# Optimization experiments

Measured on AMD Instinct MI355X. Metric: run time of the kernel, lower is better.

## Reference

```python
import jax, jax.numpy as jnp
import numpy as np

NUM_HEADS = 16


def setup_inputs() -> dict:
    key = jax.random.key(0)
    k1, k2, k3, k4 = jax.random.split(key, 4)
    B, N, C = 4, 2048, 1024
    x = jax.random.normal(k1, (B, N, C), dtype=jnp.float32)
    g_info = jax.random.normal(k2, (2, 4, C), dtype=jnp.float32)
    qkv_w = jax.random.normal(k3, (3 * C, C), dtype=jnp.float32) * 0.02
    proj_w = jax.random.normal(k4, (C, C), dtype=jnp.float32) * 0.02
    proj_b = jnp.zeros((C,), dtype=jnp.float32)
    return {"x": x, "g_info": g_info, "qkv_w": qkv_w, "proj_w": proj_w, "proj_b": proj_b}


def reference(x, g_info, qkv_w, proj_w, proj_b):
    B, N, C = x.shape
    H = NUM_HEADS
    D = C // H
    scale = D ** -0.5
    # qkv projection (no bias): [B,N,3C] -> [B,N,3,H,D]
    qkv = (x @ qkv_w.T).reshape(B, N, 3, H, D)
    q, k, v = qkv[:, :, 0], qkv[:, :, 1], qkv[:, :, 2]  # each [B,N,H,D]
    # global-info fusion: g_info[0] -> (4,H,D); rows = q_g, k_g, v_g, t_g
    gl = g_info[0].reshape(4, H, D)
    q_g = gl[0][None, None]  # [1,1,H,D]
    k_g = gl[1][None, None]
    # NOTE: source computes min/max rescaled q_g/k_g but they are dead code;
    # the attention actually uses the unscaled additive fusion below.
    q_fused = q + q_g
    k_fused = k + k_g
    # memory_efficient_attention(q,k,v): softmax(q k^T / sqrt(D)) v
    attn = jnp.einsum("bqhd,bkhd->bhqk", q_fused, k_fused) * scale
    attn = jax.nn.softmax(attn, axis=-1)
    out = jnp.einsum("bhqk,bkhd->bqhd", attn, v).reshape(B, N, C)
    out = out @ proj_w.T + proj_b
    return (out, g_info[1:])
```

## Files before the change

### kernel.cpp

```cpp
#include <hip/hip_runtime.h>

typedef _Float16 h4 __attribute__((ext_vector_type(4)));
typedef _Float16 h8 __attribute__((ext_vector_type(8)));
typedef __fp16 fp16x2 __attribute__((ext_vector_type(2)));
typedef float f4 __attribute__((ext_vector_type(4)));
typedef float f16v __attribute__((ext_vector_type(16)));

#define MFMA16(a,b,c) __builtin_amdgcn_mfma_f32_16x16x32_f16(a, b, c, 0, 0, 0)
#define MFMA32(a,b,c) __builtin_amdgcn_mfma_f32_32x32x16_f16(a, b, c, 0, 0, 0)
#define EXP2(x) __builtin_amdgcn_exp2f(x)

__device__ __forceinline__ void gload_lds16(const _Float16* g, _Float16* l) {
    __builtin_amdgcn_global_load_lds((const __attribute__((address_space(1))) void*)g,
                                     (__attribute__((address_space(3))) void*)l, 16, 0, 0);
}

__device__ __forceinline__ void half_swap(float v, float& a, float& b) {
    unsigned x = __float_as_uint(v), y = x;
    asm("v_permlane32_swap_b32 %0, %1" : "+v"(x), "+v"(y));
    a = __uint_as_float(x); b = __uint_as_float(y);
}

__device__ __forceinline__ h8 ldfrag_sw(const _Float16* S, int R, int kk, int kq) {
    int b = kk * 4 + kq;
    return *(const h8*)(S + R * 64 + ((b ^ (R & 7)) * 8));
}

__device__ __forceinline__ void gemm_main(const _Float16* __restrict__ A, const _Float16* __restrict__ B,
                                          int K, int tM, int tN, int tid,
                                          _Float16* As, _Float16* Bs, f4 acc[4][4]) {
    int lane = tid & 63, w = tid >> 6;
    int wm = w >> 1, wn = w & 1;
    int ln = lane & 15, kq = lane >> 4;
    int r = tid >> 3;
    int sb = tid & 7;

#define GSTAGE(buf, k0)                                                                     \
    {                                                                                       \
        _Pragma("unroll")                                                                   \
        for (int it = 0; it < 4; ++it) {                                                    \
            int row = r + it * 32;                                                          \
            int srcb = sb ^ (row & 7);                                                      \
            gload_lds16(A + (size_t)(tM * 128 + row) * K + (k0) + srcb * 8,                 \
                        As + (buf) * 8192 + ((tid & ~63) + it * 256) * 8);                  \
            gload_lds16(B + (size_t)(tN * 128 + row) * K + (k0) + srcb * 8,                 \
                        Bs + (buf) * 8192 + ((tid & ~63) + it * 256) * 8);                  \
        }                                                                                   \
    }

    GSTAGE(0, 0);
    __syncthreads();

    int cur = 0;
    for (int k0 = 0; k0 < K; k0 += 64) {
        if (k0 + 64 < K) GSTAGE(cur ^ 1, k0 + 64);

        const _Float16* Asc = As + cur * 8192;
        const _Float16* Bsc = Bs + cur * 8192;
        __builtin_amdgcn_s_setprio(1);
#pragma unroll
        for (int kk = 0; kk < 2; ++kk) {
            h8 af[4], bf[4];
#pragma unroll
            for (int mi = 0; mi < 4; ++mi) af[mi] = ldfrag_sw(Asc, wm * 64 + mi * 16 + ln, kk, kq);
#pragma unroll
            for (int ni = 0; ni < 4; ++ni) bf[ni] = ldfrag_sw(Bsc, wn * 64 + ni * 16 + ln, kk, kq);
#pragma unroll
            for (int mi = 0; mi < 4; ++mi)
#pragma unroll
                for (int ni = 0; ni < 4; ++ni) acc[mi][ni] = MFMA16(af[mi], bf[ni], acc[mi][ni]);
        }
        __builtin_amdgcn_s_setprio(0);
        __syncthreads();
        cur ^= 1;
    }
#undef GSTAGE
}

__global__ __launch_bounds__(256) void k_cvt3(const float* __restrict__ x, const float* __restrict__ wq,
                                              const float* __restrict__ wp, _Float16* __restrict__ xh,
                                              _Float16* __restrict__ wqh, _Float16* __restrict__ wph) {
    const int NX = 1048576, NQ = 393216, NP = 131072;
    int stride = gridDim.x * blockDim.x;
    for (int s = blockIdx.x * blockDim.x + threadIdx.x; s < NX + NQ + NP; s += stride) {
        const float* src;
        _Float16* dst;
        int off;
        if (s < NX) { src = x; dst = xh; off = s; }
        else if (s < NX + NQ) { src = wq; dst = wqh; off = s - NX; }
        else { src = wp; dst = wph; off = s - NX - NQ; }
        float4 a = ((const float4*)src)[off * 2];
        float4 b = ((const float4*)src)[off * 2 + 1];
        h8 r = {(_Float16)a.x, (_Float16)a.y, (_Float16)a.z, (_Float16)a.w,
                (_Float16)b.x, (_Float16)b.y, (_Float16)b.z, (_Float16)b.w};
        ((h8*)dst)[off] = r;
    }
}

__global__ __launch_bounds__(256) void k_qkv(const _Float16* __restrict__ A, const _Float16* __restrict__ B,
                                             const float* __restrict__ g, _Float16* __restrict__ Qf,
                                             _Float16* __restrict__ Kf, _Float16* __restrict__ Vt) {
    __shared__ __align__(16) _Float16 As[2 * 128 * 64];
    __shared__ __align__(16) _Float16 Bs[2 * 128 * 64];
    int tid = threadIdx.x;
    int tN = blockIdx.x, tM = blockIdx.y;
    int lane = tid & 63, w = tid >> 6;
    int wm = w >> 1, wn = w & 1;
    int ln = lane & 15, kq = lane >> 4;

    f4 acc[4][4] = {};
    gemm_main(A, B, 1024, tM, tN, tid, As, Bs, acc);

#pragma unroll
    for (int mi = 0; mi < 4; ++mi) {
#pragma unroll
        for (int ni = 0; ni < 4; ++ni) {
#pragma unroll
            for (int r = 0; r < 4; ++r) {
                int gr = tM * 128 + wm * 64 + mi * 16 + kq * 4 + r;
                int gc = tN * 128 + wn * 64 + ni * 16 + ln;
                float val = acc[mi][ni][r];
                int which = gc >> 10;
                int c = gc & 1023, h = c >> 6, d = c & 63;
                int b = gr >> 11, n = gr & 2047;
                int bh = b * 16 + h;
                if (which == 0) {
                    val = (val + g[c]) * 0.18033688f;
                    Qf[((size_t)bh * 2048 + n) * 64 + d] = (_Float16)val;
                } else if (which == 1) {
                    val += g[1024 + c];
                    Kf[((size_t)bh * 2048 + n) * 64 + d] = (_Float16)val;
                } else {
                    Vt[((size_t)bh * 64 + d) * 2048 + n] = (_Float16)val;
                }
            }
        }
    }
}

__global__ __launch_bounds__(256) void k_attn(const _Float16* __restrict__ Qf, const _Float16* __restrict__ Kf,
                                              const _Float16* __restrict__ Vt, _Float16* __restrict__ Oa) {
    __shared__ __align__(16) _Float16 KV[2][2][64 * 64];
    int tid = threadIdx.x;
    int qt = blockIdx.x, bh = blockIdx.y;
    int lane = tid & 63, w = tid >> 6;
    int l31 = lane & 31, hi = lane >> 5;
    const _Float16* Qb = Qf + (size_t)bh * 2048 * 64;
    const _Float16* Kb = Kf + (size_t)bh * 2048 * 64;
    const _Float16* Vb = Vt + (size_t)bh * 64 * 2048;
    int qrow0 = qt * 128 + w * 32;

    int srow = tid >> 3, sblk = tid & 7;
    int sblk0 = (sblk ^ (srow & 7)) * 8;

#define STAGE(bufi, kvc)                                                                     \
    {                                                                                        \
        _Float16* lk = &KV[bufi][0][0] + ((tid & ~63)) * 8;                                  \
        _Float16* lv = &KV[bufi][1][0] + ((tid & ~63)) * 8;                                  \
        gload_lds16(Kb + (size_t)((kvc) + srow) * 64 + sblk0, lk);                           \
        gload_lds16(Kb + (size_t)((kvc) + srow + 32) * 64 + sblk0, lk + 2048);               \
        gload_lds16(Vb + (size_t)srow * 2048 + (kvc) + sblk0, lv);                           \
        gload_lds16(Vb + (size_t)(srow + 32) * 2048 + (kvc) + sblk0, lv + 2048);             \
    }

    h8 qfr[4];
#pragma unroll
    for (int dc = 0; dc < 4; ++dc)
        qfr[dc] = *(const h8*)(Qb + (size_t)(qrow0 + l31) * 64 + dc * 16 + hi * 8);

    f16v o0 = {}, o1 = {};
    float l_run = 0.f;

    STAGE(0, 0);
    __syncthreads();

    int cur = 0;
    for (int kvc = 0; kvc < 2048; kvc += 64) {
        if (kvc + 64 < 2048) STAGE(cur ^ 1, kvc + 64);

        const _Float16* Klc = &KV[cur][0][0];
        const _Float16* Vlc = &KV[cur][1][0];
        int sw = l31 & 7;

        f16v s0, s1;
#pragma unroll
        for (int r = 0; r < 16; ++r) { s0[r] = -4.f; s1[r] = -4.f; }
        __builtin_amdgcn_s_setprio(1);
#pragma unroll
        for (int dc = 0; dc < 4; ++dc) {
            int cb = dc * 2 + hi;
            h8 kf0 = *(const h8*)&Klc[l31 * 64 + ((cb ^ sw) * 8)];
            h8 kf1 = *(const h8*)&Klc[(32 + l31) * 64 + ((cb ^ sw) * 8)];
            s0 = MFMA32(kf0, qfr[dc], s0);
            s1 = MFMA32(kf1, qfr[dc], s1);
        }
        __builtin_amdgcn_s_setprio(0);

        float ps0[16], ps1[16];
#pragma unroll
        for (int r = 0; r < 16; ++r) ps0[r] = EXP2(s0[r]);
#pragma unroll
        for (int r = 0; r < 16; ++r) ps1[r] = EXP2(s1[r]);

        float t[16];
#pragma unroll
        for (int i = 0; i < 16; ++i) t[i] = ps0[i] + ps1[i];
#pragma unroll
        for (int i = 0; i < 8; ++i) t[i] += t[i + 8];
#pragma unroll
        for (int i = 0; i < 4; ++i) t[i] += t[i + 4];
        l_run += (t[0] + t[1]) + (t[2] + t[3]);

        unsigned W[16];
#pragma unroll
        for (int i = 0; i < 8; ++i) {
            union { fp16x2 h; unsigned u; } a, b;
            a.h = __builtin_amdgcn_cvt_pkrtz(ps0[2 * i], ps0[2 * i + 1]);
            b.h = __builtin_amdgcn_cvt_pkrtz(ps1[2 * i], ps1[2 * i + 1]);
            W[i] = a.u;
            W[8 + i] = b.u;
        }

        __builtin_amdgcn_s_setprio(1);
#pragma unroll
        for (int t2 = 0; t2 < 2; ++t2) {
#pragma unroll
            for (int kcl = 0; kcl < 2; ++kcl) {
                unsigned w0 = W[t2 * 8 + kcl * 4 + 0], w1 = W[t2 * 8 + kcl * 4 + 1];
                unsigned w2 = W[t2 * 8 + kcl * 4 + 2], w3 = W[t2 * 8 + kcl * 4 + 3];
                asm("v_permlane32_swap_b32 %0, %1" : "+v"(w0), "+v"(w2));
                asm("v_permlane32_swap_b32 %0, %1" : "+v"(w1), "+v"(w3));
                union { unsigned u[4]; h8 v; } pf;
                pf.u[0] = w0; pf.u[1] = w1; pf.u[2] = w2; pf.u[3] = w3;
                int cb = (t2 * 2 + kcl) * 2 + hi;
                h8 vf0 = *(const h8*)&Vlc[l31 * 64 + ((cb ^ sw) * 8)];
                h8 vf1 = *(const h8*)&Vlc[(32 + l31) * 64 + ((cb ^ sw) * 8)];
                o0 = MFMA32(pf.v, vf0, o0);
                o1 = MFMA32(pf.v, vf1, o1);
            }
        }
        __builtin_amdgcn_s_setprio(0);

        __syncthreads();
        cur ^= 1;
    }
#undef STAGE

    float la, lb;
    half_swap(l_run, la, lb);
    float inv = 1.f / (la + lb);
    int b = bh >> 4, h = bh & 15;
#pragma unroll
    for (int r = 0; r < 16; ++r) {
        int qloc = (r & 3) + 8 * (r >> 2) + 4 * hi;
        float iv = __shfl(inv, qloc, 64);
        size_t base = ((size_t)b * 2048 + qrow0 + qloc) * 1024 + h * 64;
        Oa[base + l31] = (_Float16)(o0[r] * iv);
        Oa[base + 32 + l31] = (_Float16)(o1[r] * iv);
    }
}

__global__ __launch_bounds__(256) void k_proj(const _Float16* __restrict__ A, const _Float16* __restrict__ B,
                                              const float* __restrict__ bias, float* __restrict__ out) {
    __shared__ __align__(16) _Float16 As[2 * 128 * 64];
    __shared__ __align__(16) _Float16 Bs[2 * 128 * 64];
    int tid = threadIdx.x;
    int tN = blockIdx.x, tM = blockIdx.y;
    int lane = tid & 63, w = tid >> 6;
    int wm = w >> 1, wn = w & 1;
    int ln = lane & 15, kq = lane >> 4;

    f4 acc[4][4] = {};
    gemm_main(A, B, 1024, tM, tN, tid, As, Bs, acc);

#pragma unroll
    for (int mi = 0; mi < 4; ++mi) {
#pragma unroll
        for (int ni = 0; ni < 4; ++ni) {
#pragma unroll
            for (int r = 0; r < 4; ++r) {
                int gr = tM * 128 + wm * 64 + mi * 16 + kq * 4 + r;
                int gc = tN * 128 + wn * 64 + ni * 16 + ln;
                out[(size_t)gr * 1024 + gc] = acc[mi][ni][r] + bias[gc];
            }
        }
    }
}

__global__ __launch_bounds__(256) void k_tail(const float* __restrict__ g, float* __restrict__ out) {
    int i = blockIdx.x * 256 + threadIdx.x;
    out[i] = g[4096 + i];
}

extern "C" void kernel_launch(void* const* d_in, const int* in_sizes, int n_in,
                              void* d_out, int out_size, void* d_ws, size_t ws_size,
                              hipStream_t stream) {
    const float* x = (const float*)d_in[0];
    const float* g = (const float*)d_in[1];
    const float* wq = (const float*)d_in[2];
    const float* wp = (const float*)d_in[3];
    const float* pb = (const float*)d_in[4];
    float* out = (float*)d_out;

    _Float16* xh = (_Float16*)d_ws;
    _Float16* wqh = xh + 8388608;
    _Float16* wph = wqh + 3145728;
    _Float16* Qf = wph + 1048576;
    _Float16* Kf = Qf + 8388608;
    _Float16* Vt = Kf + 8388608;
    _Float16* Oa = xh;

    k_cvt3<<<2048, 256, 0, stream>>>(x, wq, wp, xh, wqh, wph);
    k_qkv<<<dim3(24, 64), 256, 0, stream>>>(xh, wqh, g, Qf, Kf, Vt);
    k_attn<<<dim3(16, 64), 256, 0, stream>>>(Qf, Kf, Vt, Oa);
    k_proj<<<dim3(8, 64), 256, 0, stream>>>(Oa, wph, pb, out);
    k_tail<<<16, 256, 0, stream>>>(g, out + 8388608);
}
```

Baseline: 230.9 us.

## Deepen GEMM pipeline to 4-stage ring with K=32 slices and single barrier

Restructures the shared GEMM mainloop used by the QKV and projection kernels. The old double buffer of K=64 slices with two syncthreads per step becomes a 4-buffer ring of K=32 slices, prefetching three stages ahead. Each step uses one vmcnt wait plus one barrier, and the LDS swizzle is adapted to 32-wide rows. The goal is to hide global-to-LDS latency better and cut barrier overhead, at the cost of twice as many loop iterations, each with half the MFMA work.

```diff
diff --git a/kernel.cpp b/kernel.cpp
--- a/kernel.cpp
+++ b/kernel.cpp
@@ -21,9 +21,8 @@
     a = __uint_as_float(x); b = __uint_as_float(y);
 }
 
-__device__ __forceinline__ h8 ldfrag_sw(const _Float16* S, int R, int kk, int kq) {
-    int b = kk * 4 + kq;
-    return *(const h8*)(S + R * 64 + ((b ^ (R & 7)) * 8));
+__device__ __forceinline__ h8 ldfrag32(const _Float16* S, int R, int kq) {
+    return *(const h8*)(S + R * 32 + ((kq ^ (R & 3)) * 8));
 }
 
 __device__ __forceinline__ void gemm_main(const _Float16* __restrict__ A, const _Float16* __restrict__ B,
@@ -32,49 +31,58 @@
     int lane = tid & 63, w = tid >> 6;
     int wm = w >> 1, wn = w & 1;
     int ln = lane & 15, kq = lane >> 4;
-    int r = tid >> 3;
-    int sb = tid & 7;
+    int nsteps = K >> 5;
 
 #define GSTAGE(buf, k0)                                                                     \
     {                                                                                       \
         _Pragma("unroll")                                                                   \
-        for (int it = 0; it < 4; ++it) {                                                    \
-            int row = r + it * 32;                                                          \
-            int srcb = sb ^ (row & 7);                                                      \
+        for (int it = 0; it < 2; ++it) {                                                    \
+            int slot = tid + it * 256;                                                      \
+            int row = slot >> 2, blk = slot & 3;                                            \
+            int srcb = blk ^ (row & 3);                                                     \
             gload_lds16(A + (size_t)(tM * 128 + row) * K + (k0) + srcb * 8,                 \
-                        As + (buf) * 8192 + ((tid & ~63) + it * 256) * 8);                  \
+                        As + (buf) * 4096 + ((tid & ~63) + it * 256) * 8);                  \
             gload_lds16(B + (size_t)(tN * 128 + row) * K + (k0) + srcb * 8,                 \
-                        Bs + (buf) * 8192 + ((tid & ~63) + it * 256) * 8);                  \
+                        Bs + (buf) * 4096 + ((tid & ~63) + it * 256) * 8);                  \
         }                                                                                   \
     }
 
+#define GCOMP(buf)                                                                          \
+    {                                                                                       \
+        const _Float16* Asc = As + (buf) * 4096;                                            \
+        const _Float16* Bsc = Bs + (buf) * 4096;                                            \
+        h8 af[4], bf[4];                                                                    \
+        _Pragma("unroll")                                                                   \
+        for (int mi = 0; mi < 4; ++mi) af[mi] = ldfrag32(Asc, wm * 64 + mi * 16 + ln, kq);  \
+        _Pragma("unroll")                                                                   \
+        for (int ni = 0; ni < 4; ++ni) bf[ni] = ldfrag32(Bsc, wn * 64 + ni * 16 + ln, kq);  \
+        _Pragma("unroll")                                                                   \
+        for (int mi = 0; mi < 4; ++mi)                                                      \
+            _Pragma("unroll")                                                               \
+            for (int ni = 0; ni < 4; ++ni) acc[mi][ni] = MFMA16(af[mi], bf[ni], acc[mi][ni]); \
+    }
+
     GSTAGE(0, 0);
-    __syncthreads();
-
-    int cur = 0;
-    for (int k0 = 0; k0 < K; k0 += 64) {
-        if (k0 + 64 < K) GSTAGE(cur ^ 1, k0 + 64);
-
-        const _Float16* Asc = As + cur * 8192;
-        const _Float16* Bsc = Bs + cur * 8192;
+    GSTAGE(1, 32);
+    GSTAGE(2, 64);
+
+    for (int k = 0; k < nsteps - 2; ++k) {
+        asm volatile("s_waitcnt vmcnt(8)" ::: "memory");
+        __builtin_amdgcn_s_barrier();
+        if (k < nsteps - 3) GSTAGE((k + 3) & 3, (k + 3) * 32);
         __builtin_amdgcn_s_setprio(1);
-#pragma unroll
-        for (int kk = 0; kk < 2; ++kk) {
-            h8 af[4], bf[4];
-#pragma unroll
-            for (int mi = 0; mi < 4; ++mi) af[mi] = ldfrag_sw(Asc, wm * 64 + mi * 16 + ln, kk, kq);
-#pragma unroll
-            for (int ni = 0; ni < 4; ++ni) bf[ni] = ldfrag_sw(Bsc, wn * 64 + ni * 16 + ln, kk, kq);
-#pragma unroll
-            for (int mi = 0; mi < 4; ++mi)
-#pragma unroll
-                for (int ni = 0; ni < 4; ++ni) acc[mi][ni] = MFMA16(af[mi], bf[ni], acc[mi][ni]);
-        }
+        GCOMP(k & 3);
         __builtin_amdgcn_s_setprio(0);
-        __syncthreads();
-        cur ^= 1;
+    }
+    for (int k = nsteps - 2; k < nsteps; ++k) {
+        asm volatile("s_waitcnt vmcnt(0)" ::: "memory");
+        __builtin_amdgcn_s_barrier();
+        __builtin_amdgcn_s_setprio(1);
+        GCOMP(k & 3);
+        __builtin_amdgcn_s_setprio(0);
     }
 #undef GSTAGE
+#undef GCOMP
 }
 
 __global__ __launch_bounds__(256) void k_cvt3(const float* __restrict__ x, const float* __restrict__ wq,
@@ -100,8 +108,8 @@
 __global__ __launch_bounds__(256) void k_qkv(const _Float16* __restrict__ A, const _Float16* __restrict__ B,
                                              const float* __restrict__ g, _Float16* __restrict__ Qf,
                                              _Float16* __restrict__ Kf, _Float16* __restrict__ Vt) {
-    __shared__ __align__(16) _Float16 As[2 * 128 * 64];
-    __shared__ __align__(16) _Float16 Bs[2 * 128 * 64];
+    __shared__ __align__(16) _Float16 As[4 * 128 * 32];
+    __shared__ __align__(16) _Float16 Bs[4 * 128 * 32];
     int tid = threadIdx.x;
     int tN = blockIdx.x, tM = blockIdx.y;
     int lane = tid & 63, w = tid >> 6;
@@ -262,8 +270,8 @@
 
 __global__ __launch_bounds__(256) void k_proj(const _Float16* __restrict__ A, const _Float16* __restrict__ B,
                                               const float* __restrict__ bias, float* __restrict__ out) {
-    __shared__ __align__(16) _Float16 As[2 * 128 * 64];
-    __shared__ __align__(16) _Float16 Bs[2 * 128 * 64];
+    __shared__ __align__(16) _Float16 As[4 * 128 * 32];
+    __shared__ __align__(16) _Float16 Bs[4 * 128 * 32];
     int tid = threadIdx.x;
     int tN = blockIdx.x, tM = blockIdx.y;
     int lane = tid & 63, w = tid >> 6;
```

Result: slower. 247.3 us (+7.1%).
